# Performance work log

Measured on AMD Instinct MI355X. Metric: run time of the kernel, lower is better.

The kernel has to match this reference:

```python
import jax, jax.numpy as jnp
import numpy as np

EMBED_DIM = 1024
NUM_HEADS = 16
HEAD_DIM = EMBED_DIM // NUM_HEADS


def setup_inputs() -> dict:
    key = jax.random.key(0)
    ks = jax.random.split(key, 6)
    B, S, D = 2, 2048, EMBED_DIM
    x = jax.random.normal(ks[0], (B, S, D), dtype=jnp.float32)
    # qkv linear: weight [3D, D] (torch layout), bias [3D]
    w_qkv = jax.random.normal(ks[1], (3 * D, D), dtype=jnp.float32) * (1.0 / np.sqrt(D))
    b_qkv = jax.random.normal(ks[2], (3 * D,), dtype=jnp.float32) * 0.01
    # projection linear: weight [D, D], bias [D]
    w_proj = jax.random.normal(ks[3], (D, D), dtype=jnp.float32) * (1.0 / np.sqrt(D))
    b_proj = jax.random.normal(ks[4], (D,), dtype=jnp.float32) * 0.01
    # per-head LayerNorm params over head_dim
    q_gamma = jnp.ones((HEAD_DIM,), jnp.float32)
    q_beta = jnp.zeros((HEAD_DIM,), jnp.float32)
    k_gamma = jnp.ones((HEAD_DIM,), jnp.float32)
    k_beta = jnp.zeros((HEAD_DIM,), jnp.float32)
    return {"x": x, "w_qkv": w_qkv, "b_qkv": b_qkv, "w_proj": w_proj,
            "b_proj": b_proj, "q_gamma": q_gamma, "q_beta": q_beta,
            "k_gamma": k_gamma, "k_beta": k_beta}


def _layernorm(x, gamma, beta, eps=1e-5):
    mu = jnp.mean(x, axis=-1, keepdims=True)
    var = jnp.mean(jnp.square(x - mu), axis=-1, keepdims=True)
    return (x - mu) * jax.lax.rsqrt(var + eps) * gamma + beta


def reference(x, w_qkv, b_qkv, w_proj, b_proj, q_gamma, q_beta, k_gamma, k_beta):
    B, S, D = x.shape
    H, Hd = NUM_HEADS, HEAD_DIM
    qkv = x @ w_qkv.T + b_qkv                     # [B, S, 3D]
    qkv = qkv.reshape(B, S, 3, H, Hd)
    q = qkv[:, :, 0].transpose(0, 2, 1, 3)        # [B, H, S, Hd]
    k = qkv[:, :, 1].transpose(0, 2, 1, 3)
    v = qkv[:, :, 2].transpose(0, 2, 1, 3)
    q = _layernorm(q, q_gamma, q_beta)
    k = _layernorm(k, k_gamma, k_beta)
    scale = 1.0 / np.sqrt(Hd).astype(np.float32)
    attn = jnp.einsum('bhqd,bhkd->bhqk', q, k) * scale
    attn = jax.nn.softmax(attn, axis=-1)
    out = jnp.einsum('bhqk,bhkd->bhqd', attn, v)  # [B, H, S, Hd]
    out = out.transpose(0, 2, 1, 3).reshape(B, S, D)
    out = out @ w_proj.T + b_proj
    # projection_dropout: identity in eval / p=0.0
    return out
```

## Files before the change

kernel.cpp:

```cpp
#include <hip/hip_runtime.h>
#include <hip/hip_bf16.h>


typedef __attribute__((ext_vector_type(8)))  short bf16x8;
typedef __attribute__((ext_vector_type(4)))  float f32x4;
typedef __attribute__((ext_vector_type(16))) float f32x16;

__device__ __forceinline__ unsigned short f2bf(float f) {
  union { float f; unsigned u; } v; v.f = f;
  unsigned r = v.u + 0x7FFFu + ((v.u >> 16) & 1u);
  return (unsigned short)(r >> 16);
}

__device__ __forceinline__ unsigned pkbf(float a, float b) {
  unsigned r;
  asm("v_cvt_pk_bf16_f32 %0, %1, %2" : "=v"(r) : "v"(a), "v"(b));
  return r;
}

__device__ __forceinline__ void pl32swap(unsigned& x, unsigned& y) {
  asm("v_permlane32_swap_b32 %0, %1" : "+v"(x), "+v"(y));
}

__device__ __forceinline__ float fexp2(float x) {
  float r; asm("v_exp_f32 %0, %1" : "=v"(r) : "v"(x)); return r;
}

__device__ __forceinline__ void gld_lds16(const void* g, void* l) {
  __builtin_amdgcn_global_load_lds(
      (const __attribute__((address_space(1))) void*)g,
      (__attribute__((address_space(3))) void*)l, 16, 0, 0);
}

__global__ __launch_bounds__(256) void k_cvt3(const float* __restrict__ x,
                                              const float* __restrict__ wq,
                                              const float* __restrict__ wp,
                                              unsigned short* __restrict__ d) {
  int i = blockIdx.x * 256 + threadIdx.x;
  const float* s;
  int off;
  if (i < 1048576)      { s = x;  off = i; }
  else if (i < 1835008) { s = wq; off = i - 1048576; }
  else                  { s = wp; off = i - 1835008; }
  float4 v = ((const float4*)s)[off];
  ushort4 o;
  o.x = f2bf(v.x); o.y = f2bf(v.y); o.z = f2bf(v.z); o.w = f2bf(v.w);
  ((ushort4*)d)[i] = o;
}

template<int BM, int BN, int WM, int WN>
__global__ __launch_bounds__(256) void k_gemm(
    const unsigned short* __restrict__ A, const unsigned short* __restrict__ B,
    const float* __restrict__ bias, float* __restrict__ C, int M, int N, int K)
{
  constexpr int FM = BM / WM / 16;
  constexpr int FN = BN / WN / 16;
  __shared__ unsigned short lA[BM * 64];
  __shared__ unsigned short lB[BN * 64];
  int tid = threadIdx.x;
  int lane = tid & 63, wid = tid >> 6;
  int lg = lane >> 4, lo = lane & 15;
  int wm = wid / WN, wn = wid % WN;
  int m0 = blockIdx.y * BM, n0 = blockIdx.x * BN;

  f32x4 acc[FM][FN];
#pragma unroll
  for (int i = 0; i < FM; ++i)
#pragma unroll
    for (int j = 0; j < FN; ++j) acc[i][j] = (f32x4){0.f, 0.f, 0.f, 0.f};

  const int srow = tid >> 3, scol = (tid & 7) * 8;

  for (int kt = 0; kt < K; kt += 64) {
    __syncthreads();
#pragma unroll
    for (int i = 0; i < BM / 32; ++i)
      gld_lds16(A + (size_t)(m0 + srow + 32 * i) * K + kt + scol,
                &lA[(srow + 32 * i) * 64 + scol]);
#pragma unroll
    for (int i = 0; i < BN / 32; ++i)
      gld_lds16(B + (size_t)(n0 + srow + 32 * i) * K + kt + scol,
                &lB[(srow + 32 * i) * 64 + scol]);
    __syncthreads();

#pragma unroll
    for (int ks = 0; ks < 2; ++ks) {
      bf16x8 af[FM], bfr[FN];
#pragma unroll
      for (int i = 0; i < FM; ++i)
        af[i] = *(const bf16x8*)&lA[(wm * (BM / WM) + i * 16 + lo) * 64 + ks * 32 + lg * 8];
#pragma unroll
      for (int j = 0; j < FN; ++j)
        bfr[j] = *(const bf16x8*)&lB[(wn * (BN / WN) + j * 16 + lo) * 64 + ks * 32 + lg * 8];
      __builtin_amdgcn_s_setprio(1);
#pragma unroll
      for (int i = 0; i < FM; ++i)
#pragma unroll
        for (int j = 0; j < FN; ++j)
          acc[i][j] = __builtin_amdgcn_mfma_f32_16x16x32_bf16(af[i], bfr[j], acc[i][j], 0, 0, 0);
      __builtin_amdgcn_s_setprio(0);
    }
  }

#pragma unroll
  for (int j = 0; j < FN; ++j) {
    int col = n0 + wn * (BN / WN) + j * 16 + lo;
    float bb = bias[col];
#pragma unroll
    for (int i = 0; i < FM; ++i)
#pragma unroll
      for (int r = 0; r < 4; ++r) {
        int row = m0 + wm * (BM / WM) + i * 16 + lg * 4 + r;
        C[(size_t)row * N + col] = acc[i][j][r] + bb;
      }
  }
}

__global__ __launch_bounds__(256) void k_gemm_qkv(
    const unsigned short* __restrict__ A,
    const unsigned short* __restrict__ B,
    const float* __restrict__ bias,
    const float* __restrict__ qg, const float* __restrict__ qb,
    const float* __restrict__ kg, const float* __restrict__ kb,
    unsigned short* __restrict__ qh,
    unsigned short* __restrict__ kh,
    unsigned short* __restrict__ vf)
{
  __shared__ unsigned short lA[128 * 64];
  __shared__ unsigned short lB[128 * 64];
  int tid = threadIdx.x;
  int lane = tid & 63, wid = tid >> 6;
  int lg = lane >> 4, lo = lane & 15;
  int wm = wid >> 1, wn = wid & 1;
  int m0 = blockIdx.y * 128, n0 = blockIdx.x * 128;
  const int K = 1024;

  f32x4 acc[4][4];
#pragma unroll
  for (int i = 0; i < 4; ++i)
#pragma unroll
    for (int j = 0; j < 4; ++j) acc[i][j] = (f32x4){0.f, 0.f, 0.f, 0.f};

  const int srow = tid >> 3, scol = (tid & 7) * 8;

  for (int kt = 0; kt < K; kt += 64) {
    __syncthreads();
#pragma unroll
    for (int i = 0; i < 4; ++i)
      gld_lds16(A + (size_t)(m0 + srow + 32 * i) * K + kt + scol,
                &lA[(srow + 32 * i) * 64 + scol]);
#pragma unroll
    for (int i = 0; i < 4; ++i)
      gld_lds16(B + (size_t)(n0 + srow + 32 * i) * K + kt + scol,
                &lB[(srow + 32 * i) * 64 + scol]);
    __syncthreads();

#pragma unroll
    for (int ks = 0; ks < 2; ++ks) {
      bf16x8 af[4], bfr[4];
#pragma unroll
      for (int i = 0; i < 4; ++i)
        af[i] = *(const bf16x8*)&lA[(wm * 64 + i * 16 + lo) * 64 + ks * 32 + lg * 8];
#pragma unroll
      for (int j = 0; j < 4; ++j)
        bfr[j] = *(const bf16x8*)&lB[(wn * 64 + j * 16 + lo) * 64 + ks * 32 + lg * 8];
      __builtin_amdgcn_s_setprio(1);
#pragma unroll
      for (int i = 0; i < 4; ++i)
#pragma unroll
        for (int j = 0; j < 4; ++j)
          acc[i][j] = __builtin_amdgcn_mfma_f32_16x16x32_bf16(af[i], bfr[j], acc[i][j], 0, 0, 0);
      __builtin_amdgcn_s_setprio(0);
    }
  }

  int m0b = m0 & 2047;
  int bb_ = m0 >> 11;
  int hcol = (n0 + wn * 64) >> 6;
  float bias4[4];
#pragma unroll
  for (int j = 0; j < 4; ++j) bias4[j] = bias[n0 + wn * 64 + j * 16 + lo];

  if (hcol >= 32) {
    int bh = bb_ * 16 + (hcol - 32);
    int T = m0b >> 7;
    int hi_ = lg >> 1;
    int j8b = (lg & 1) * 4;
    unsigned short* vbase = vf + (size_t)bh * 131072 + T * 8192 + hi_ * 256 + j8b;
#pragma unroll
    for (int i = 0; i < 4; ++i) {
      int ss = wm * 4 + i;
#pragma unroll
      for (int j = 0; j < 4; ++j) {
        int dh = j >> 1, dp = (j & 1) * 16 + lo;
        uint2 w;
        w.x = pkbf(acc[i][j][0] + bias4[j], acc[i][j][1] + bias4[j]);
        w.y = pkbf(acc[i][j][2] + bias4[j], acc[i][j][3] + bias4[j]);
        *(uint2*)(vbase + ss * 1024 + dh * 512 + dp * 8) = w;
      }
    }
  } else {
    bool isq = hcol < 16;
    int bh = bb_ * 16 + (isq ? hcol : hcol - 16);
    const float* g = isq ? qg : kg;
    const float* bt = isq ? qb : kb;
    float osc = isq ? 0.18033688f : 1.0f;
    float g4[4], t4[4];
#pragma unroll
    for (int j = 0; j < 4; ++j) {
      g4[j] = g[j * 16 + lo] * osc;
      t4[j] = bt[j * 16 + lo] * osc;
    }
    unsigned short* dst = (isq ? qh : kh) + (size_t)bh * 131072;
#pragma unroll
    for (int i = 0; i < 4; ++i) {
#pragma unroll
      for (int r = 0; r < 4; ++r) {
        float v0 = acc[i][0][r] + bias4[0];
        float v1 = acc[i][1][r] + bias4[1];
        float v2 = acc[i][2][r] + bias4[2];
        float v3 = acc[i][3][r] + bias4[3];
        float sm = (v0 + v1) + (v2 + v3);
        sm += __shfl_xor(sm, 1, 64); sm += __shfl_xor(sm, 2, 64);
        sm += __shfl_xor(sm, 4, 64); sm += __shfl_xor(sm, 8, 64);
        float mu = sm * (1.0f / 64.0f);
        float d0 = v0 - mu, d1 = v1 - mu, d2 = v2 - mu, d3 = v3 - mu;
        float vv = (d0 * d0 + d1 * d1) + (d2 * d2 + d3 * d3);
        vv += __shfl_xor(vv, 1, 64); vv += __shfl_xor(vv, 2, 64);
        vv += __shfl_xor(vv, 4, 64); vv += __shfl_xor(vv, 8, 64);
        float rs = rsqrtf(vv * (1.0f / 64.0f) + 1e-5f);
        int s = m0b + wm * 64 + i * 16 + lg * 4 + r;
        unsigned short* row = dst + (size_t)s * 64 + lo;
        row[0]  = f2bf(fmaf(d0 * rs, g4[0], t4[0]));
        row[16] = f2bf(fmaf(d1 * rs, g4[1], t4[1]));
        row[32] = f2bf(fmaf(d2 * rs, g4[2], t4[2]));
        row[48] = f2bf(fmaf(d3 * rs, g4[3], t4[3]));
      }
    }
  }
}

__global__ __launch_bounds__(256, 3) void k_attn(
    const unsigned short* __restrict__ Q,
    const unsigned short* __restrict__ K,
    const unsigned short* __restrict__ VF,
    unsigned short* __restrict__ O)
{
  __shared__ char lK[2][16384];

  int tid = threadIdx.x;
  int wid = tid >> 6, lane = tid & 63;
  int l31 = lane & 31, hi = lane >> 5;
  int qc = wid >> 1, g = wid & 1;

  int id = blockIdx.x;
  int nid = (id & 7) * 128 + (id >> 3);
  int bh = nid >> 5;
  int q0 = (nid & 31) << 6;
  int q = q0 + qc * 32 + l31;

  const unsigned short* qp = Q + ((size_t)bh * 2048 + q) * 64 + hi * 8;
  bf16x8 qf[4];
#pragma unroll
  for (int s = 0; s < 4; ++s) qf[s] = *(const bf16x8*)(qp + 16 * s);

  const char* kbytes = (const char*)(K + (size_t)bh * 131072);
  const unsigned short* vfb = VF + (size_t)bh * 131072 + lane * 8;

  f32x16 z16;
#pragma unroll
  for (int i = 0; i < 16; ++i) z16[i] = 0.f;
  float m = -1e30f, lsum = 0.0f;
  f32x16 o0 = z16, o1 = z16;

#pragma unroll
  for (int ii = 0; ii < 4; ++ii) {
    int b = ii * 4096 + tid * 16;
    int sb = b ^ (((b >> 7) & 7) << 4);
    gld_lds16(kbytes + sb, &lK[0][b]);
  }
  __syncthreads();

  int pb = 0;
  for (int i = 0; i < 16; ++i) {
    const char* bK = &lK[pb][g * 8192];
    const unsigned short* vt = vfb + (size_t)(2 * i + g) * 4096;

    bf16x8 vv[8];
#pragma unroll
    for (int s = 0; s < 4; ++s) {
      vv[2 * s]     = *(const bf16x8*)(vt + s * 1024);
      vv[2 * s + 1] = *(const bf16x8*)(vt + s * 1024 + 512);
    }
    __builtin_amdgcn_sched_barrier(0);

    if (i < 15) {
#pragma unroll
      for (int ii = 0; ii < 4; ++ii) {
        int b = ii * 4096 + tid * 16;
        int sb = b ^ (((b >> 7) & 7) << 4);
        gld_lds16(kbytes + (size_t)(i + 1) * 16384 + sb, &lK[pb ^ 1][b]);
      }
    }

    f32x16 sc[2];
    __builtin_amdgcn_s_setprio(1);
#pragma unroll
    for (int c = 0; c < 2; ++c) {
      int row = c * 32 + l31;
      int rx = (row * 128) ^ ((row & 7) << 4);
      bf16x8 kf = *(const bf16x8*)(bK + (rx ^ (hi * 16)));
      sc[c] = __builtin_amdgcn_mfma_f32_32x32x16_bf16(kf, qf[0], z16, 0, 0, 0);
#pragma unroll
      for (int s = 1; s < 4; ++s) {
        kf = *(const bf16x8*)(bK + (rx ^ ((2 * s + hi) * 16)));
        sc[c] = __builtin_amdgcn_mfma_f32_32x32x16_bf16(kf, qf[s], sc[c], 0, 0, 0);
      }
    }
    __builtin_amdgcn_s_setprio(0);

    float r[8];
#pragma unroll
    for (int i2 = 0; i2 < 8; ++i2)
      r[i2] = fmaxf(fmaxf(sc[0][i2], sc[0][i2 + 8]),
                    fmaxf(sc[1][i2], sc[1][i2 + 8]));
    float pm = fmaxf(fmaxf(fmaxf(r[0], r[1]), fmaxf(r[2], r[3])),
                     fmaxf(fmaxf(r[4], r[5]), fmaxf(r[6], r[7])));
    pm = fmaxf(pm, __shfl_xor(pm, 32, 64));

    if (!__all(pm - m <= 8.0f)) {
      float mn = fmaxf(m, pm);
      float fac = fexp2(m - mn);
      m = mn;
      lsum *= fac;
#pragma unroll
      for (int i2 = 0; i2 < 16; ++i2) { o0[i2] *= fac; o1[i2] *= fac; }
    }

#pragma unroll
    for (int c = 0; c < 2; ++c)
#pragma unroll
      for (int i2 = 0; i2 < 16; ++i2) sc[c][i2] = fexp2(sc[c][i2] - m);
    float ts[16];
#pragma unroll
    for (int i2 = 0; i2 < 16; ++i2) ts[i2] = sc[0][i2] + sc[1][i2];
#pragma unroll
    for (int d = 8; d; d >>= 1)
#pragma unroll
      for (int i2 = 0; i2 < d; ++i2) ts[i2] += ts[i2 + d];
    lsum += ts[0] + __shfl_xor(ts[0], 32, 64);

#pragma unroll
    for (int s = 0; s < 4; ++s) {
      const f32x16& sf = sc[s >> 1];
      const int rb = (s & 1) * 8;
      unsigned d0 = pkbf(sf[rb + 0], sf[rb + 1]);
      unsigned d1 = pkbf(sf[rb + 2], sf[rb + 3]);
      unsigned d2 = pkbf(sf[rb + 4], sf[rb + 5]);
      unsigned d3 = pkbf(sf[rb + 6], sf[rb + 7]);
      pl32swap(d0, d2);
      pl32swap(d1, d3);
      union { unsigned u[4]; bf16x8 v; } pu;
      pu.u[0] = d0; pu.u[1] = d1; pu.u[2] = d2; pu.u[3] = d3;
      __builtin_amdgcn_s_setprio(1);
      o0 = __builtin_amdgcn_mfma_f32_32x32x16_bf16(vv[2 * s],     pu.v, o0, 0, 0, 0);
      o1 = __builtin_amdgcn_mfma_f32_32x32x16_bf16(vv[2 * s + 1], pu.v, o1, 0, 0, 0);
      __builtin_amdgcn_s_setprio(0);
    }

    __syncthreads();
    pb ^= 1;
  }

  float* mb = (float*)&lK[0][0];
  int base = (qc * 64 + lane) * 34;
  if (g) {
#pragma unroll
    for (int i2 = 0; i2 < 16; ++i2) { mb[base + i2] = o0[i2]; mb[base + 16 + i2] = o1[i2]; }
    mb[base + 32] = m; mb[base + 33] = lsum;
  }
  __syncthreads();
  if (!g) {
    float m1 = mb[base + 32], l1 = mb[base + 33];
    float mn = fmaxf(m, m1);
    float f0 = fexp2(m - mn), f1 = fexp2(m1 - mn);
    float linv = 1.0f / (lsum * f0 + l1 * f1);
    float a0 = f0 * linv, a1 = f1 * linv;
    int b = bh >> 4, h = bh & 15;
    unsigned short* ob = O + ((size_t)(b * 2048 + q)) * 1024 + h * 64;
#pragma unroll
    for (int gg = 0; gg < 4; ++gg) {
      uint2 w;
      w.x = pkbf(o0[4 * gg + 0] * a0 + mb[base + 4 * gg + 0] * a1,
                 o0[4 * gg + 1] * a0 + mb[base + 4 * gg + 1] * a1);
      w.y = pkbf(o0[4 * gg + 2] * a0 + mb[base + 4 * gg + 2] * a1,
                 o0[4 * gg + 3] * a0 + mb[base + 4 * gg + 3] * a1);
      *(uint2*)(ob + 8 * gg + 4 * hi) = w;
      w.x = pkbf(o1[4 * gg + 0] * a0 + mb[base + 16 + 4 * gg + 0] * a1,
                 o1[4 * gg + 1] * a0 + mb[base + 16 + 4 * gg + 1] * a1);
      w.y = pkbf(o1[4 * gg + 2] * a0 + mb[base + 16 + 4 * gg + 2] * a1,
                 o1[4 * gg + 3] * a0 + mb[base + 16 + 4 * gg + 3] * a1);
      *(uint2*)(ob + 32 + 8 * gg + 4 * hi) = w;
    }
  }
}

extern "C" void kernel_launch(void* const* d_in, const int* in_sizes, int n_in,
                              void* d_out, int out_size, void* d_ws, size_t ws_size,
                              hipStream_t stream)
{
  (void)in_sizes; (void)n_in; (void)out_size; (void)ws_size;
  const float* x      = (const float*)d_in[0];
  const float* w_qkv  = (const float*)d_in[1];
  const float* b_qkv  = (const float*)d_in[2];
  const float* w_proj = (const float*)d_in[3];
  const float* b_proj = (const float*)d_in[4];
  const float* q_g    = (const float*)d_in[5];
  const float* q_b    = (const float*)d_in[6];
  const float* k_g    = (const float*)d_in[7];
  const float* k_b    = (const float*)d_in[8];
  float* out = (float*)d_out;

  char* p = (char*)d_ws;
  unsigned short* x_bf  = (unsigned short*)p;  p += (size_t)4096 * 1024 * 2;
  unsigned short* wq_bf = (unsigned short*)p;  p += (size_t)3072 * 1024 * 2;
  unsigned short* wp_bf = (unsigned short*)p;  p += (size_t)1024 * 1024 * 2;
  unsigned short* qh    = (unsigned short*)p;  p += (size_t)32 * 2048 * 64 * 2;
  unsigned short* kh    = (unsigned short*)p;  p += (size_t)32 * 2048 * 64 * 2;
  unsigned short* vfr   = (unsigned short*)p;  p += (size_t)32 * 131072 * 2;
  unsigned short* ao    = (unsigned short*)p;  p += (size_t)4096 * 1024 * 2;

  k_cvt3<<<8192, 256, 0, stream>>>(x, w_qkv, w_proj, x_bf);

  k_gemm_qkv<<<dim3(24, 32), 256, 0, stream>>>(x_bf, wq_bf, b_qkv,
                                               q_g, q_b, k_g, k_b, qh, kh, vfr);
  k_attn<<<1024, 256, 0, stream>>>(qh, kh, vfr, ao);
  k_gemm<64, 128, 1, 4><<<dim3(8, 64), 256, 0, stream>>>(ao, wp_bf, b_proj, out, 4096, 1024, 1024);
}
```

Before: 137.8 us.

## Software-pipeline QK^T of next K tile with softmax and PV of previous

Restructures the attention main loop so the QK^T MFMAs for the next K tile are issued before the softmax and PV work of the previous tile, using two score buffers and a loop unrolled by two over the double-buffered LDS K tiles. This is meant to overlap matrix-core work with the exp/max/sum vector work and so cut idle MFMA time. V fragments are now loaded inside the PV step instead of being prefetched at the top of the iteration, which may expose global-load latency. Keeping two live score accumulators raises register pressure under the 3-waves launch bound, with a risk of spills or reduced occupancy.

Measured after the change: 154.4 us (median of 5 runs). +12.0%, slower.

```diff
diff --git a/kernel.cpp b/kernel.cpp
--- a/kernel.cpp
+++ b/kernel.cpp
@@ -240,6 +240,93 @@
   }
 }
 
+
+__device__ __forceinline__ void stage_pair(const char* kbytes, int pair,
+                                           char* dst, int tid) {
+#pragma unroll
+  for (int ii = 0; ii < 4; ++ii) {
+    int b = ii * 4096 + tid * 16;
+    int sb = b ^ (((b >> 7) & 7) << 4);
+    gld_lds16(kbytes + (size_t)pair * 16384 + sb, dst + b);
+  }
+}
+
+__device__ __forceinline__ void qk_body(f32x16 (&sc)[2], const char* lKbuf,
+                                        int g, int l31, int hi,
+                                        const bf16x8 (&qf)[4], const f32x16& z16) {
+  const char* bK = lKbuf + g * 8192;
+  __builtin_amdgcn_s_setprio(1);
+#pragma unroll
+  for (int c = 0; c < 2; ++c) {
+    int row = c * 32 + l31;
+    int rx = (row * 128) ^ ((row & 7) << 4);
+    bf16x8 kf = *(const bf16x8*)(bK + (rx ^ (hi * 16)));
+    sc[c] = __builtin_amdgcn_mfma_f32_32x32x16_bf16(kf, qf[0], z16, 0, 0, 0);
+#pragma unroll
+    for (int s = 1; s < 4; ++s) {
+      kf = *(const bf16x8*)(bK + (rx ^ ((2 * s + hi) * 16)));
+      sc[c] = __builtin_amdgcn_mfma_f32_32x32x16_bf16(kf, qf[s], sc[c], 0, 0, 0);
+    }
+  }
+  __builtin_amdgcn_s_setprio(0);
+}
+
+__device__ __forceinline__ void smpv_body(f32x16 (&sc)[2],
+                                          const unsigned short* vt,
+                                          float& m, float& lsum,
+                                          f32x16& o0, f32x16& o1) {
+  float r[8];
+#pragma unroll
+  for (int i2 = 0; i2 < 8; ++i2)
+    r[i2] = fmaxf(fmaxf(sc[0][i2], sc[0][i2 + 8]),
+                  fmaxf(sc[1][i2], sc[1][i2 + 8]));
+  float pm = fmaxf(fmaxf(fmaxf(r[0], r[1]), fmaxf(r[2], r[3])),
+                   fmaxf(fmaxf(r[4], r[5]), fmaxf(r[6], r[7])));
+  pm = fmaxf(pm, __shfl_xor(pm, 32, 64));
+
+  if (!__all(pm - m <= 8.0f)) {
+    float mn = fmaxf(m, pm);
+    float fac = fexp2(m - mn);
+    m = mn;
+    lsum *= fac;
+#pragma unroll
+    for (int i2 = 0; i2 < 16; ++i2) { o0[i2] *= fac; o1[i2] *= fac; }
+  }
+
+#pragma unroll
+  for (int c = 0; c < 2; ++c)
+#pragma unroll
+    for (int i2 = 0; i2 < 16; ++i2) sc[c][i2] = fexp2(sc[c][i2] - m);
+  float ts[16];
+#pragma unroll
+  for (int i2 = 0; i2 < 16; ++i2) ts[i2] = sc[0][i2] + sc[1][i2];
+#pragma unroll
+  for (int d = 8; d; d >>= 1)
+#pragma unroll
+    for (int i2 = 0; i2 < d; ++i2) ts[i2] += ts[i2 + d];
+  lsum += ts[0] + __shfl_xor(ts[0], 32, 64);
+
+#pragma unroll
+  for (int s = 0; s < 4; ++s) {
+    const f32x16& sf = sc[s >> 1];
+    const int rb = (s & 1) * 8;
+    unsigned d0 = pkbf(sf[rb + 0], sf[rb + 1]);
+    unsigned d1 = pkbf(sf[rb + 2], sf[rb + 3]);
+    unsigned d2 = pkbf(sf[rb + 4], sf[rb + 5]);
+    unsigned d3 = pkbf(sf[rb + 6], sf[rb + 7]);
+    pl32swap(d0, d2);
+    pl32swap(d1, d3);
+    union { unsigned u[4]; bf16x8 v; } pu;
+    pu.u[0] = d0; pu.u[1] = d1; pu.u[2] = d2; pu.u[3] = d3;
+    bf16x8 v0 = *(const bf16x8*)(vt + s * 1024);
+    bf16x8 v1 = *(const bf16x8*)(vt + s * 1024 + 512);
+    __builtin_amdgcn_s_setprio(1);
+    o0 = __builtin_amdgcn_mfma_f32_32x32x16_bf16(v0, pu.v, o0, 0, 0, 0);
+    o1 = __builtin_amdgcn_mfma_f32_32x32x16_bf16(v1, pu.v, o1, 0, 0, 0);
+    __builtin_amdgcn_s_setprio(0);
+  }
+}
+
 __global__ __launch_bounds__(256, 3) void k_attn(
     const unsigned short* __restrict__ Q,
     const unsigned short* __restrict__ K,
@@ -273,104 +360,29 @@
   float m = -1e30f, lsum = 0.0f;
   f32x16 o0 = z16, o1 = z16;
 
-#pragma unroll
-  for (int ii = 0; ii < 4; ++ii) {
-    int b = ii * 4096 + tid * 16;
-    int sb = b ^ (((b >> 7) & 7) << 4);
-    gld_lds16(kbytes + sb, &lK[0][b]);
-  }
+  f32x16 scA[2], scB[2];
+
+  stage_pair(kbytes, 0, lK[0], tid);
   __syncthreads();
-
-  int pb = 0;
-  for (int i = 0; i < 16; ++i) {
-    const char* bK = &lK[pb][g * 8192];
-    const unsigned short* vt = vfb + (size_t)(2 * i + g) * 4096;
-
-    bf16x8 vv[8];
-#pragma unroll
-    for (int s = 0; s < 4; ++s) {
-      vv[2 * s]     = *(const bf16x8*)(vt + s * 1024);
-      vv[2 * s + 1] = *(const bf16x8*)(vt + s * 1024 + 512);
-    }
-    __builtin_amdgcn_sched_barrier(0);
-
-    if (i < 15) {
-#pragma unroll
-      for (int ii = 0; ii < 4; ++ii) {
-        int b = ii * 4096 + tid * 16;
-        int sb = b ^ (((b >> 7) & 7) << 4);
-        gld_lds16(kbytes + (size_t)(i + 1) * 16384 + sb, &lK[pb ^ 1][b]);
-      }
-    }
-
-    f32x16 sc[2];
-    __builtin_amdgcn_s_setprio(1);
-#pragma unroll
-    for (int c = 0; c < 2; ++c) {
-      int row = c * 32 + l31;
-      int rx = (row * 128) ^ ((row & 7) << 4);
-      bf16x8 kf = *(const bf16x8*)(bK + (rx ^ (hi * 16)));
-      sc[c] = __builtin_amdgcn_mfma_f32_32x32x16_bf16(kf, qf[0], z16, 0, 0, 0);
-#pragma unroll
-      for (int s = 1; s < 4; ++s) {
-        kf = *(const bf16x8*)(bK + (rx ^ ((2 * s + hi) * 16)));
-        sc[c] = __builtin_amdgcn_mfma_f32_32x32x16_bf16(kf, qf[s], sc[c], 0, 0, 0);
-      }
-    }
-    __builtin_amdgcn_s_setprio(0);
-
-    float r[8];
-#pragma unroll
-    for (int i2 = 0; i2 < 8; ++i2)
-      r[i2] = fmaxf(fmaxf(sc[0][i2], sc[0][i2 + 8]),
-                    fmaxf(sc[1][i2], sc[1][i2 + 8]));
-    float pm = fmaxf(fmaxf(fmaxf(r[0], r[1]), fmaxf(r[2], r[3])),
-                     fmaxf(fmaxf(r[4], r[5]), fmaxf(r[6], r[7])));
-    pm = fmaxf(pm, __shfl_xor(pm, 32, 64));
-
-    if (!__all(pm - m <= 8.0f)) {
-      float mn = fmaxf(m, pm);
-      float fac = fexp2(m - mn);
-      m = mn;
-      lsum *= fac;
-#pragma unroll
-      for (int i2 = 0; i2 < 16; ++i2) { o0[i2] *= fac; o1[i2] *= fac; }
-    }
-
-#pragma unroll
-    for (int c = 0; c < 2; ++c)
-#pragma unroll
-      for (int i2 = 0; i2 < 16; ++i2) sc[c][i2] = fexp2(sc[c][i2] - m);
-    float ts[16];
-#pragma unroll
-    for (int i2 = 0; i2 < 16; ++i2) ts[i2] = sc[0][i2] + sc[1][i2];
-#pragma unroll
-    for (int d = 8; d; d >>= 1)
-#pragma unroll
-      for (int i2 = 0; i2 < d; ++i2) ts[i2] += ts[i2 + d];
-    lsum += ts[0] + __shfl_xor(ts[0], 32, 64);
-
-#pragma unroll
-    for (int s = 0; s < 4; ++s) {
-      const f32x16& sf = sc[s >> 1];
-      const int rb = (s & 1) * 8;
-      unsigned d0 = pkbf(sf[rb + 0], sf[rb + 1]);
-      unsigned d1 = pkbf(sf[rb + 2], sf[rb + 3]);
-      unsigned d2 = pkbf(sf[rb + 4], sf[rb + 5]);
-      unsigned d3 = pkbf(sf[rb + 6], sf[rb + 7]);
-      pl32swap(d0, d2);
-      pl32swap(d1, d3);
-      union { unsigned u[4]; bf16x8 v; } pu;
-      pu.u[0] = d0; pu.u[1] = d1; pu.u[2] = d2; pu.u[3] = d3;
-      __builtin_amdgcn_s_setprio(1);
-      o0 = __builtin_amdgcn_mfma_f32_32x32x16_bf16(vv[2 * s],     pu.v, o0, 0, 0, 0);
-      o1 = __builtin_amdgcn_mfma_f32_32x32x16_bf16(vv[2 * s + 1], pu.v, o1, 0, 0, 0);
-      __builtin_amdgcn_s_setprio(0);
-    }
-
-    __syncthreads();
-    pb ^= 1;
-  }
+  stage_pair(kbytes, 1, lK[1], tid);
+  qk_body(scA, lK[0], g, l31, hi, qf, z16);
+  __syncthreads();
+
+#pragma unroll 1
+  for (int ii = 0; ii < 7; ++ii) {
+    stage_pair(kbytes, 2 * ii + 2, lK[0], tid);
+    qk_body(scB, lK[1], g, l31, hi, qf, z16);
+    smpv_body(scA, vfb + (size_t)(4 * ii + g) * 4096, m, lsum, o0, o1);
+    __syncthreads();
+    stage_pair(kbytes, 2 * ii + 3, lK[1], tid);
+    qk_body(scA, lK[0], g, l31, hi, qf, z16);
+    smpv_body(scB, vfb + (size_t)(4 * ii + 2 + g) * 4096, m, lsum, o0, o1);
+    __syncthreads();
+  }
+
+  qk_body(scB, lK[1], g, l31, hi, qf, z16);
+  smpv_body(scA, vfb + (size_t)(28 + g) * 4096, m, lsum, o0, o1);
+  smpv_body(scB, vfb + (size_t)(30 + g) * 4096, m, lsum, o0, o1);
 
   float* mb = (float*)&lK[0][0];
   int base = (qc * 64 + lane) * 34;
```

## Double-buffer LDS tiles in GEMM kernels to overlap loads with MFMA

Applied to the files above, without the earlier changes.

Both the generic GEMM and the fused QKV GEMM move from a single 64-wide K tile to two ping-pong 32-wide K tiles in shared memory. The next tile's global-to-LDS load is issued before the MFMAs on the current tile, and only one barrier is kept per iteration. This aims to hide global memory latency behind compute. The cost is twice as many iterations and barriers for the same K, with less work per barrier. Correctness relies on the async LDS loads completing before the end-of-iteration barrier.

Result: faster. 126.1 us (-8.5%).

```diff
diff --git a/kernel.cpp b/kernel.cpp
--- a/kernel.cpp
+++ b/kernel.cpp
@@ -55,8 +55,8 @@
 {
   constexpr int FM = BM / WM / 16;
   constexpr int FN = BN / WN / 16;
-  __shared__ unsigned short lA[BM * 64];
-  __shared__ unsigned short lB[BN * 64];
+  __shared__ unsigned short lA[2][BM * 32];
+  __shared__ unsigned short lB[2][BN * 32];
   int tid = threadIdx.x;
   int lane = tid & 63, wid = tid >> 6;
   int lg = lane >> 4, lo = lane & 15;
@@ -69,37 +69,50 @@
 #pragma unroll
     for (int j = 0; j < FN; ++j) acc[i][j] = (f32x4){0.f, 0.f, 0.f, 0.f};
 
-  const int srow = tid >> 3, scol = (tid & 7) * 8;
-
-  for (int kt = 0; kt < K; kt += 64) {
+  const int srow = tid >> 2, scol = (tid & 3) * 8;
+
+#pragma unroll
+  for (int i = 0; i < BM / 64; ++i)
+    gld_lds16(A + (size_t)(m0 + srow + 64 * i) * K + scol,
+              &lA[0][(srow + 64 * i) * 32 + scol]);
+#pragma unroll
+  for (int i = 0; i < BN / 64; ++i)
+    gld_lds16(B + (size_t)(n0 + srow + 64 * i) * K + scol,
+              &lB[0][(srow + 64 * i) * 32 + scol]);
+  __syncthreads();
+
+  const int NT = K / 32;
+  int pb = 0;
+  for (int t = 0; t < NT; ++t) {
+    if (t < NT - 1) {
+      int kt = (t + 1) * 32;
+#pragma unroll
+      for (int i = 0; i < BM / 64; ++i)
+        gld_lds16(A + (size_t)(m0 + srow + 64 * i) * K + kt + scol,
+                  &lA[pb ^ 1][(srow + 64 * i) * 32 + scol]);
+#pragma unroll
+      for (int i = 0; i < BN / 64; ++i)
+        gld_lds16(B + (size_t)(n0 + srow + 64 * i) * K + kt + scol,
+                  &lB[pb ^ 1][(srow + 64 * i) * 32 + scol]);
+    }
+
+    bf16x8 af[FM], bfr[FN];
+#pragma unroll
+    for (int i = 0; i < FM; ++i)
+      af[i] = *(const bf16x8*)&lA[pb][(wm * (BM / WM) + i * 16 + lo) * 32 + lg * 8];
+#pragma unroll
+    for (int j = 0; j < FN; ++j)
+      bfr[j] = *(const bf16x8*)&lB[pb][(wn * (BN / WN) + j * 16 + lo) * 32 + lg * 8];
+    __builtin_amdgcn_s_setprio(1);
+#pragma unroll
+    for (int i = 0; i < FM; ++i)
+#pragma unroll
+      for (int j = 0; j < FN; ++j)
+        acc[i][j] = __builtin_amdgcn_mfma_f32_16x16x32_bf16(af[i], bfr[j], acc[i][j], 0, 0, 0);
+    __builtin_amdgcn_s_setprio(0);
+
     __syncthreads();
-#pragma unroll
-    for (int i = 0; i < BM / 32; ++i)
-      gld_lds16(A + (size_t)(m0 + srow + 32 * i) * K + kt + scol,
-                &lA[(srow + 32 * i) * 64 + scol]);
-#pragma unroll
-    for (int i = 0; i < BN / 32; ++i)
-      gld_lds16(B + (size_t)(n0 + srow + 32 * i) * K + kt + scol,
-                &lB[(srow + 32 * i) * 64 + scol]);
-    __syncthreads();
-
-#pragma unroll
-    for (int ks = 0; ks < 2; ++ks) {
-      bf16x8 af[FM], bfr[FN];
-#pragma unroll
-      for (int i = 0; i < FM; ++i)
-        af[i] = *(const bf16x8*)&lA[(wm * (BM / WM) + i * 16 + lo) * 64 + ks * 32 + lg * 8];
-#pragma unroll
-      for (int j = 0; j < FN; ++j)
-        bfr[j] = *(const bf16x8*)&lB[(wn * (BN / WN) + j * 16 + lo) * 64 + ks * 32 + lg * 8];
-      __builtin_amdgcn_s_setprio(1);
-#pragma unroll
-      for (int i = 0; i < FM; ++i)
-#pragma unroll
-        for (int j = 0; j < FN; ++j)
-          acc[i][j] = __builtin_amdgcn_mfma_f32_16x16x32_bf16(af[i], bfr[j], acc[i][j], 0, 0, 0);
-      __builtin_amdgcn_s_setprio(0);
-    }
+    pb ^= 1;
   }
 
 #pragma unroll
@@ -126,8 +139,8 @@
     unsigned short* __restrict__ kh,
     unsigned short* __restrict__ vf)
 {
-  __shared__ unsigned short lA[128 * 64];
-  __shared__ unsigned short lB[128 * 64];
+  __shared__ unsigned short lA[2][128 * 32];
+  __shared__ unsigned short lB[2][128 * 32];
   int tid = threadIdx.x;
   int lane = tid & 63, wid = tid >> 6;
   int lg = lane >> 4, lo = lane & 15;
@@ -141,37 +154,47 @@
 #pragma unroll
     for (int j = 0; j < 4; ++j) acc[i][j] = (f32x4){0.f, 0.f, 0.f, 0.f};
 
-  const int srow = tid >> 3, scol = (tid & 7) * 8;
-
-  for (int kt = 0; kt < K; kt += 64) {
+  const int srow = tid >> 2, scol = (tid & 3) * 8;
+
+#pragma unroll
+  for (int i = 0; i < 2; ++i) {
+    gld_lds16(A + (size_t)(m0 + srow + 64 * i) * K + scol,
+              &lA[0][(srow + 64 * i) * 32 + scol]);
+    gld_lds16(B + (size_t)(n0 + srow + 64 * i) * K + scol,
+              &lB[0][(srow + 64 * i) * 32 + scol]);
+  }
+  __syncthreads();
+
+  int pb = 0;
+  for (int t = 0; t < 32; ++t) {
+    if (t < 31) {
+      int kt = (t + 1) * 32;
+#pragma unroll
+      for (int i = 0; i < 2; ++i) {
+        gld_lds16(A + (size_t)(m0 + srow + 64 * i) * K + kt + scol,
+                  &lA[pb ^ 1][(srow + 64 * i) * 32 + scol]);
+        gld_lds16(B + (size_t)(n0 + srow + 64 * i) * K + kt + scol,
+                  &lB[pb ^ 1][(srow + 64 * i) * 32 + scol]);
+      }
+    }
+
+    bf16x8 af[4], bfr[4];
+#pragma unroll
+    for (int i = 0; i < 4; ++i)
+      af[i] = *(const bf16x8*)&lA[pb][(wm * 64 + i * 16 + lo) * 32 + lg * 8];
+#pragma unroll
+    for (int j = 0; j < 4; ++j)
+      bfr[j] = *(const bf16x8*)&lB[pb][(wn * 64 + j * 16 + lo) * 32 + lg * 8];
+    __builtin_amdgcn_s_setprio(1);
+#pragma unroll
+    for (int i = 0; i < 4; ++i)
+#pragma unroll
+      for (int j = 0; j < 4; ++j)
+        acc[i][j] = __builtin_amdgcn_mfma_f32_16x16x32_bf16(af[i], bfr[j], acc[i][j], 0, 0, 0);
+    __builtin_amdgcn_s_setprio(0);
+
     __syncthreads();
-#pragma unroll
-    for (int i = 0; i < 4; ++i)
-      gld_lds16(A + (size_t)(m0 + srow + 32 * i) * K + kt + scol,
-                &lA[(srow + 32 * i) * 64 + scol]);
-#pragma unroll
-    for (int i = 0; i < 4; ++i)
-      gld_lds16(B + (size_t)(n0 + srow + 32 * i) * K + kt + scol,
-                &lB[(srow + 32 * i) * 64 + scol]);
-    __syncthreads();
-
-#pragma unroll
-    for (int ks = 0; ks < 2; ++ks) {
-      bf16x8 af[4], bfr[4];
-#pragma unroll
-      for (int i = 0; i < 4; ++i)
-        af[i] = *(const bf16x8*)&lA[(wm * 64 + i * 16 + lo) * 64 + ks * 32 + lg * 8];
-#pragma unroll
-      for (int j = 0; j < 4; ++j)
-        bfr[j] = *(const bf16x8*)&lB[(wn * 64 + j * 16 + lo) * 64 + ks * 32 + lg * 8];
-      __builtin_amdgcn_s_setprio(1);
-#pragma unroll
-      for (int i = 0; i < 4; ++i)
-#pragma unroll
-        for (int j = 0; j < 4; ++j)
-          acc[i][j] = __builtin_amdgcn_mfma_f32_16x16x32_bf16(af[i], bfr[j], acc[i][j], 0, 0, 0);
-      __builtin_amdgcn_s_setprio(0);
-    }
+    pb ^= 1;
   }
 
   int m0b = m0 & 2047;
```
